# Performance work log

Measured on AMD Instinct MI355X. Metric: run time of the kernel, lower is better.

## Reference

```python
import jax, jax.numpy as jnp
import numpy as np

LEN_HIS = 20   # q_len_his: sliding-window history length
DIM_C = 4      # dim_c
H = 64         # GRU hidden = final_mlp_hidden_width
D = 36         # global_graph_width(32) + goal(2) + action(2)
N = 32768      # total timesteps across many episodes


def setup_inputs() -> dict:
    key = jax.random.key(0)
    ks = jax.random.split(key, 8)
    emb = jax.random.normal(ks[0], (N, D), jnp.float32)
    dones = (jax.random.uniform(ks[1], (N, 1)) < 0.02).astype(jnp.int32)
    s = lambda k, shape, fan: jax.random.normal(k, shape, jnp.float32) / np.sqrt(fan).astype(np.float32)
    return {
        "embeddings": emb,
        "W_ih": s(ks[2], (3 * H, D), D),
        "W_hh": s(ks[3], (3 * H, H), H),
        "b_ih": jnp.zeros((3 * H,), jnp.float32),
        "b_hh": jnp.zeros((3 * H,), jnp.float32),
        "W1": s(ks[4], (H, H), H),
        "b1": jnp.zeros((H,), jnp.float32),
        "W2": s(ks[5], (DIM_C, H), H),
        "b2": jnp.zeros((DIM_C,), jnp.float32),
        "dones": dones,
    }


def _his_calculate_c(embeddings, W_ih, W_hh, b_ih, b_hh, W1, b1, W2, b2, dones):
    """Batched/padded version of the ragged sliding-window GRU+MLP loop.

    For each timestep t, the torch code runs the GRU over
    embeddings[max(episode_start, t-L+1) : t+1] from a zero hidden state,
    then applies FinalPredMLP to the final hidden state.
    """
    n = embeddings.shape[0]
    done = dones[:, 0] != 0
    idx = jnp.arange(n)
    # episode_start[t] = (index of most recent done strictly before t) + 1, else 0
    prev_done = jnp.concatenate([jnp.zeros((1,), bool), done[:-1]])
    ep_start = jax.lax.cummax(jnp.where(prev_done, idx, 0))
    win_start = jnp.maximum(ep_start, idx - LEN_HIS + 1)            # [N]

    # padded windows: position l holds embeddings[t - (L-1) + l]
    gidx = idx[:, None] - (LEN_HIS - 1) + jnp.arange(LEN_HIS)[None, :]  # [N, L]
    valid = gidx >= win_start[:, None]                                   # [N, L]
    X = embeddings[jnp.clip(gidx, 0, n - 1)] * valid[..., None]          # [N, L, D]

    def cell(h, inp):
        x, v = inp                      # x: [N, D], v: [N]
        gi = x @ W_ih.T + b_ih          # [N, 3H]
        gh = h @ W_hh.T + b_hh          # [N, 3H]
        ir, iz, inn = jnp.split(gi, 3, axis=-1)
        hr, hz, hnn = jnp.split(gh, 3, axis=-1)
        r = jax.nn.sigmoid(ir + hr)
        z = jax.nn.sigmoid(iz + hz)
        ncand = jnp.tanh(inn + r * hnn)
        h_new = (1.0 - z) * ncand + z * h
        return jnp.where(v[:, None], h_new, h), None

    h0 = jnp.zeros((n, H), embeddings.dtype)
    hT, _ = jax.lax.scan(cell, h0, (jnp.swapaxes(X, 0, 1), valid.T))  # [N, H]

    # FinalPredMLP: Linear(H,H) -> ReLU -> Linear(H, dim_c)
    hid = jax.nn.relu(hT @ W1.T + b1)
    return hid @ W2.T + b2              # [N, dim_c]


def reference(embeddings, W_ih, W_hh, b_ih, b_hh, W1, b1, W2, b2, dones):
    return _his_calculate_c(embeddings, W_ih, W_hh, b_ih, b_hh, W1, b1, W2, b2, dones)
```

## Files before the change

kernel.cpp:

```cpp
#include <hip/hip_runtime.h>

#define NT 32768
#define DI 36
#define HH 64
#define LH 20
#define TPB 64
#define NROW 83
#define SGS 196
#define EMBS 40

#define NLOG2E -1.4426950408889634f
#define TLOG2E 2.8853900817779268f

#define UNION_OFF  65072
#define SFIRST_OFF 78352
#define SMEM_BYTES 78608

typedef __attribute__((ext_vector_type(8))) short bf16x8;
typedef __attribute__((ext_vector_type(4))) float f32x4;
typedef __attribute__((ext_vector_type(4))) int int4v;
union frag_cast { int4v i4; bf16x8 h8; };

__device__ __forceinline__ unsigned f2u(float f) { union { float f; unsigned u; } x; x.f = f; return x.u; }
__device__ __forceinline__ float u2f(unsigned u) { union { float f; unsigned u; } x; x.u = u; return x.f; }
__device__ __forceinline__ unsigned short f2bf_rne(float f) {
    union { float f; unsigned u; } x; x.f = f;
    unsigned r = x.u + 0x7FFFu + ((x.u >> 16) & 1u);
    return (unsigned short)(r >> 16);
}

__device__ __forceinline__ void gate4(const f32x4 aR, const f32x4 aZ,
                                      const f32x4 aI, const f32x4 aN,
                                      const bool valid, float* hh) {
    float dR[4], dZ[4], dN[4], rv[4], zv[4], iv[4];
#pragma unroll
    for (int e = 0; e < 4; ++e) dR[e] = 1.f + __builtin_amdgcn_exp2f(aR[e]);
#pragma unroll
    for (int e = 0; e < 4; ++e) dZ[e] = 1.f + __builtin_amdgcn_exp2f(aZ[e]);
    {
        const float pa = dR[0] * dR[1], pb = dR[2] * dR[3];
        const float rp = __builtin_amdgcn_rcpf(pa * pb);
        const float ia = rp * pb, ib = rp * pa;
        rv[0] = ia * dR[1]; rv[1] = ia * dR[0];
        rv[2] = ib * dR[3]; rv[3] = ib * dR[2];
    }
    {
        const float pa = dZ[0] * dZ[1], pb = dZ[2] * dZ[3];
        const float rp = __builtin_amdgcn_rcpf(pa * pb);
        const float ia = rp * pb, ib = rp * pa;
        zv[0] = ia * dZ[1]; zv[1] = ia * dZ[0];
        zv[2] = ib * dZ[3]; zv[3] = ib * dZ[2];
    }
#pragma unroll
    for (int e = 0; e < 4; ++e)
        dN[e] = 1.f + __builtin_amdgcn_exp2f(fmaf(rv[e], aN[e], aI[e]));
    {
        const float pa = dN[0] * dN[1], pb = dN[2] * dN[3];
        const float rp = __builtin_amdgcn_rcpf(pa * pb);
        const float ia = rp * pb, ib = rp * pa;
        iv[0] = ia * dN[1]; iv[1] = ia * dN[0];
        iv[2] = ib * dN[3]; iv[3] = ib * dN[2];
    }
#pragma unroll
    for (int e = 0; e < 4; ++e) {
        const float nc = fmaf(-2.f, iv[e], 1.f);
        const float hn = fmaf(zv[e], hh[e] - nc, nc);
        hh[e] = valid ? hn : hh[e];
    }
}

__global__ __launch_bounds__(64) void prep_kernel(
    const float* __restrict__ W_ih, const float* __restrict__ W_hh,
    const float* __restrict__ W1, int4v* __restrict__ wfrag)
{
    const int b = (int)blockIdx.x;
    const int l = (int)threadIdx.x;
    unsigned short e[8];
    if (b < 72) {
        const int set = b / 24, fb = b % 24;
        const int mt = fb >> 1, kt = fb & 1;
        const int m = mt * 16 + (l & 15);
        const float sc = ((mt >> 2) < 2) ? NLOG2E : TLOG2E;
        const int k0 = kt * 32 + (l >> 4) * 8;
#pragma unroll
        for (int jj = 0; jj < 8; ++jj) {
            const int k = k0 + jj;
            if (set == 2) {
                e[jj] = f2bf_rne(W_hh[(size_t)m * HH + k] * sc);
            } else {
                const float v = (k < DI) ? W_ih[(size_t)m * DI + k] * sc : 0.f;
                const unsigned u = f2u(v);
                if (set == 0) e[jj] = (unsigned short)(u >> 16);
                else          e[jj] = (unsigned short)(f2u(v - u2f(u & 0xFFFF0000u)) >> 16);
            }
        }
    } else {
        const int bb = b - 72;
        const bool is_lo = bb >= 8;
        const int f = bb & 7;
        const int mt = f >> 1, kt = f & 1;
        const int m = mt * 16 + (l & 15);
        const int k0 = kt * 32 + (l >> 4) * 8;
#pragma unroll
        for (int jj = 0; jj < 8; ++jj) {
            const float v = W1[(size_t)m * HH + k0 + jj];
            const unsigned u = f2u(v);
            if (!is_lo) e[jj] = (unsigned short)(u >> 16);
            else        e[jj] = (unsigned short)(f2u(v - u2f(u & 0xFFFF0000u)) >> 16);
        }
    }
    int4v p;
    p.x = e[0] | ((unsigned)e[1] << 16); p.y = e[2] | ((unsigned)e[3] << 16);
    p.z = e[4] | ((unsigned)e[5] << 16); p.w = e[6] | ((unsigned)e[7] << 16);
    wfrag[b * 64 + l] = p;
}

__global__ __launch_bounds__(256, 2) void gru_kernel(
    const float* __restrict__ emb, const int4v* __restrict__ wfrag,
    const float* __restrict__ b_ih, const float* __restrict__ b_hh,
    const float* __restrict__ b1, const float* __restrict__ W2,
    const float* __restrict__ b2, const int* __restrict__ dones,
    float* __restrict__ out)
{
    __shared__ __align__(16) char SMEM[SMEM_BYTES];
    float* const Sg = (float*)SMEM;
    unsigned short* const EmbH = (unsigned short*)(SMEM + UNION_OFF);
    unsigned short* const EmbL = EmbH + NROW * EMBS;
    unsigned short* const Hb   = (unsigned short*)(SMEM + UNION_OFF);
    int* const sfirst = (int*)(SMEM + SFIRST_OFF);

    const int tid = threadIdx.x;
    const int lane = tid & 63;
    const int W = tid >> 6;
    const int li = lane & 15;
    const int q = lane >> 4;
    const int blk = ((int)blockIdx.x & 7) * 64 + ((int)blockIdx.x >> 3);
    const int T0 = blk * TPB;

    if (tid < TPB) {
        const int tt = T0 + tid;
        int off = (tt >= LH - 1) ? 0 : (LH - 1) - tt;
#pragma unroll
        for (int k = LH - 1; k >= 1; --k) {
            const int j = tt - k;
            const int jj = j < 0 ? 0 : j;
            const bool d = (j >= 0) && (dones[jj] != 0);
            if (d) off = LH - k;
        }
        sfirst[tid] = off;
    }
    for (int i = tid; i < NROW * 9; i += 256) {
        const int r = i / 9, c = i - r * 9;
        int tt = T0 - (LH - 1) + r; tt = tt < 0 ? 0 : tt;
        const f32x4 v = *(const f32x4*)&emb[(size_t)tt * DI + 4 * c];
        const unsigned u0 = f2u(v[0]), u1 = f2u(v[1]);
        const unsigned u2 = f2u(v[2]), u3 = f2u(v[3]);
        uint2 ph, pl;
        ph.x = __builtin_amdgcn_perm(u1, u0, 0x07060302u);
        ph.y = __builtin_amdgcn_perm(u3, u2, 0x07060302u);
        const unsigned l0 = f2u(v[0] - u2f(u0 & 0xFFFF0000u));
        const unsigned l1 = f2u(v[1] - u2f(u1 & 0xFFFF0000u));
        const unsigned l2 = f2u(v[2] - u2f(u2 & 0xFFFF0000u));
        const unsigned l3 = f2u(v[3] - u2f(u3 & 0xFFFF0000u));
        pl.x = __builtin_amdgcn_perm(l1, l0, 0x07060302u);
        pl.y = __builtin_amdgcn_perm(l3, l2, 0x07060302u);
        *(uint2*)&EmbH[r * EMBS + 4 * c] = ph;
        *(uint2*)&EmbL[r * EMBS + 4 * c] = pl;
    }
    if (tid < NROW) {
        const uint2 z2 = {0u, 0u};
        *(uint2*)&EmbH[tid * EMBS + DI] = z2;
        *(uint2*)&EmbL[tid * EMBS + DI] = z2;
    }

    bf16x8 aih[3][2], ail[3][2];
#pragma unroll
    for (int g = 0; g < 3; ++g)
#pragma unroll
        for (int kt = 0; kt < 2; ++kt) {
            const int fb = (4 * g + W) * 2 + kt;
            frag_cast a, b;
            a.i4 = wfrag[(0 * 24 + fb) * 64 + lane];
            b.i4 = wfrag[(1 * 24 + fb) * 64 + lane];
            aih[g][kt] = a.h8; ail[g][kt] = b.h8;
        }
    bf16x8 whh[3][4][2];
#pragma unroll
    for (int g = 0; g < 3; ++g)
#pragma unroll
        for (int mt = 0; mt < 4; ++mt)
#pragma unroll
            for (int kt = 0; kt < 2; ++kt) {
                frag_cast c;
                c.i4 = wfrag[(48 + (4 * g + mt) * 2 + kt) * 64 + lane];
                whh[g][mt][kt] = c.h8;
            }

    const int joff = 16 * W + 4 * q;
    f32x4 biasI[3];
#pragma unroll
    for (int g = 0; g < 3; ++g) {
        const float sc = (g < 2) ? NLOG2E : TLOG2E;
        const f32x4 bi = *(const f32x4*)&b_ih[64 * g + joff];
        if (g < 2) {
            const f32x4 bh = *(const f32x4*)&b_hh[64 * g + joff];
#pragma unroll
            for (int rr = 0; rr < 4; ++rr) biasI[g][rr] = (bi[rr] + bh[rr]) * sc;
        } else {
#pragma unroll
            for (int rr = 0; rr < 4; ++rr) biasI[g][rr] = bi[rr] * sc;
        }
    }
    __syncthreads();

#pragma unroll
    for (int rt = 0; rt < 6; ++rt) {
        const int row0 = (rt == 5) ? 67 : 16 * rt;
        const int row = row0 + li;
        bf16x8 ebh0 = *(const bf16x8*)&EmbH[row * EMBS + 8 * q];
        bf16x8 ebl0 = *(const bf16x8*)&EmbL[row * EMBS + 8 * q];
        bf16x8 ebh1 = bf16x8{0, 0, 0, 0, 0, 0, 0, 0};
        bf16x8 ebl1 = bf16x8{0, 0, 0, 0, 0, 0, 0, 0};
        if (q == 0) {
            ebh1 = *(const bf16x8*)&EmbH[row * EMBS + 32];
            ebl1 = *(const bf16x8*)&EmbL[row * EMBS + 32];
        }
#pragma unroll
        for (int g = 0; g < 3; ++g) {
            f32x4 a = biasI[g];
            a = __builtin_amdgcn_mfma_f32_16x16x32_bf16(aih[g][0], ebh0, a, 0, 0, 0);
            a = __builtin_amdgcn_mfma_f32_16x16x32_bf16(aih[g][1], ebh1, a, 0, 0, 0);
            a = __builtin_amdgcn_mfma_f32_16x16x32_bf16(ail[g][0], ebh0, a, 0, 0, 0);
            a = __builtin_amdgcn_mfma_f32_16x16x32_bf16(ail[g][1], ebh1, a, 0, 0, 0);
            a = __builtin_amdgcn_mfma_f32_16x16x32_bf16(aih[g][0], ebl0, a, 0, 0, 0);
            a = __builtin_amdgcn_mfma_f32_16x16x32_bf16(aih[g][1], ebl1, a, 0, 0, 0);
            *(f32x4*)&Sg[row * SGS + 64 * g + joff] = a;
        }
    }
    __syncthreads();

    f32x4 bnv4[4];
#pragma unroll
    for (int mt = 0; mt < 4; ++mt) {
        const f32x4 b = *(const f32x4*)&b_hh[128 + 16 * mt + 4 * q];
#pragma unroll
        for (int rr = 0; rr < 4; ++rr) bnv4[mt][rr] = b[rr] * TLOG2E;
    }
    const int sfr = sfirst[16 * W + li];
    unsigned short* const Hbw = Hb + W * 1152;

    float h[4][4];
    f32x4 gvR[4], gvZ[4], gvI[4];
    {
        const float* gp = Sg + (16 * W + li) * SGS;
        const bool valid = (0 >= sfr);
#pragma unroll
        for (int mt = 0; mt < 4; ++mt) {
            const f32x4 aR = *(const f32x4*)(gp + 16 * mt + 4 * q);
            const f32x4 aZ = *(const f32x4*)(gp + 64 + 16 * mt + 4 * q);
            const f32x4 aI = *(const f32x4*)(gp + 128 + 16 * mt + 4 * q);
            h[mt][0] = 0.f; h[mt][1] = 0.f; h[mt][2] = 0.f; h[mt][3] = 0.f;
            gate4(aR, aZ, aI, bnv4[mt], valid, h[mt]);
            uint2 ph;
            ph.x = __builtin_amdgcn_perm(f2u(h[mt][1]), f2u(h[mt][0]), 0x07060302u);
            ph.y = __builtin_amdgcn_perm(f2u(h[mt][3]), f2u(h[mt][2]), 0x07060302u);
            *(uint2*)&Hbw[li * 72 + 16 * mt + 4 * q] = ph;
        }
        const float* gq = Sg + (16 * W + li + 1) * SGS;
#pragma unroll
        for (int mt = 0; mt < 4; ++mt) {
            gvR[mt] = *(const f32x4*)(gq + 16 * mt + 4 * q);
            gvZ[mt] = *(const f32x4*)(gq + 64 + 16 * mt + 4 * q);
            gvI[mt] = *(const f32x4*)(gq + 128 + 16 * mt + 4 * q);
        }
    }

#pragma unroll 2
    for (int s = 1; s < LH; ++s) {
        const bf16x8 bh0 = *(const bf16x8*)&Hbw[li * 72 + 8 * q];
        const bf16x8 bh1 = *(const bf16x8*)&Hbw[li * 72 + 32 + 8 * q];
        f32x4 aR[4], aZ[4], aN[4], aI[4];
#pragma unroll
        for (int mt = 0; mt < 4; ++mt) {
            aR[mt] = gvR[mt]; aZ[mt] = gvZ[mt]; aI[mt] = gvI[mt]; aN[mt] = bnv4[mt];
        }
        {
            int rrow = 16 * W + li + s + 1; rrow = rrow > NROW - 1 ? NROW - 1 : rrow;
            const float* gq = Sg + rrow * SGS;
#pragma unroll
            for (int mt = 0; mt < 4; ++mt) {
                gvR[mt] = *(const f32x4*)(gq + 16 * mt + 4 * q);
                gvZ[mt] = *(const f32x4*)(gq + 64 + 16 * mt + 4 * q);
                gvI[mt] = *(const f32x4*)(gq + 128 + 16 * mt + 4 * q);
            }
        }
        const bool valid = (s >= sfr);
#pragma unroll
        for (int mt = 0; mt < 4; ++mt) {
            aR[mt] = __builtin_amdgcn_mfma_f32_16x16x32_bf16(whh[0][mt][0], bh0, aR[mt], 0, 0, 0);
            aR[mt] = __builtin_amdgcn_mfma_f32_16x16x32_bf16(whh[0][mt][1], bh1, aR[mt], 0, 0, 0);
            aZ[mt] = __builtin_amdgcn_mfma_f32_16x16x32_bf16(whh[1][mt][0], bh0, aZ[mt], 0, 0, 0);
            aZ[mt] = __builtin_amdgcn_mfma_f32_16x16x32_bf16(whh[1][mt][1], bh1, aZ[mt], 0, 0, 0);
            aN[mt] = __builtin_amdgcn_mfma_f32_16x16x32_bf16(whh[2][mt][0], bh0, aN[mt], 0, 0, 0);
            aN[mt] = __builtin_amdgcn_mfma_f32_16x16x32_bf16(whh[2][mt][1], bh1, aN[mt], 0, 0, 0);
            gate4(aR[mt], aZ[mt], aI[mt], aN[mt], valid, h[mt]);
            if (s != LH - 1) {
                uint2 ph;
                ph.x = __builtin_amdgcn_perm(f2u(h[mt][1]), f2u(h[mt][0]), 0x07060302u);
                ph.y = __builtin_amdgcn_perm(f2u(h[mt][3]), f2u(h[mt][2]), 0x07060302u);
                *(uint2*)&Hbw[li * 72 + 16 * mt + 4 * q] = ph;
            }
        }
    }

    bf16x8 w1h[4][2], w1l[4][2];
#pragma unroll
    for (int mt = 0; mt < 4; ++mt)
#pragma unroll
        for (int kt = 0; kt < 2; ++kt) {
            frag_cast a, b;
            a.i4 = wfrag[(72 + mt * 2 + kt) * 64 + lane];
            b.i4 = wfrag[(80 + mt * 2 + kt) * 64 + lane];
            w1h[mt][kt] = a.h8; w1l[mt][kt] = b.h8;
        }
#pragma unroll
    for (int mt = 0; mt < 4; ++mt) {
        uint2 ph;
        ph.x = __builtin_amdgcn_perm(f2u(h[mt][1]), f2u(h[mt][0]), 0x07060302u);
        ph.y = __builtin_amdgcn_perm(f2u(h[mt][3]), f2u(h[mt][2]), 0x07060302u);
        *(uint2*)&Hbw[li * 72 + 16 * mt + 4 * q] = ph;
    }
    const bf16x8 bh0 = *(const bf16x8*)&Hbw[li * 72 + 8 * q];
    const bf16x8 bh1 = *(const bf16x8*)&Hbw[li * 72 + 32 + 8 * q];
#pragma unroll
    for (int mt = 0; mt < 4; ++mt) {
        const unsigned u0 = f2u(h[mt][0]), u1 = f2u(h[mt][1]);
        const unsigned u2 = f2u(h[mt][2]), u3 = f2u(h[mt][3]);
        const unsigned l0 = f2u(h[mt][0] - u2f(u0 & 0xFFFF0000u));
        const unsigned l1 = f2u(h[mt][1] - u2f(u1 & 0xFFFF0000u));
        const unsigned l2 = f2u(h[mt][2] - u2f(u2 & 0xFFFF0000u));
        const unsigned l3 = f2u(h[mt][3] - u2f(u3 & 0xFFFF0000u));
        uint2 pl;
        pl.x = __builtin_amdgcn_perm(l1, l0, 0x07060302u);
        pl.y = __builtin_amdgcn_perm(l3, l2, 0x07060302u);
        *(uint2*)&Hbw[li * 72 + 16 * mt + 4 * q] = pl;
    }
    const bf16x8 bl0 = *(const bf16x8*)&Hbw[li * 72 + 8 * q];
    const bf16x8 bl1 = *(const bf16x8*)&Hbw[li * 72 + 32 + 8 * q];

    float p0 = 0.f, p1 = 0.f, p2 = 0.f, p3 = 0.f;
#pragma unroll
    for (int mt = 0; mt < 4; ++mt) {
        f32x4 a = *(const f32x4*)&b1[16 * mt + 4 * q];
        a = __builtin_amdgcn_mfma_f32_16x16x32_bf16(w1h[mt][0], bh0, a, 0, 0, 0);
        a = __builtin_amdgcn_mfma_f32_16x16x32_bf16(w1h[mt][1], bh1, a, 0, 0, 0);
        a = __builtin_amdgcn_mfma_f32_16x16x32_bf16(w1l[mt][0], bh0, a, 0, 0, 0);
        a = __builtin_amdgcn_mfma_f32_16x16x32_bf16(w1l[mt][1], bh1, a, 0, 0, 0);
        a = __builtin_amdgcn_mfma_f32_16x16x32_bf16(w1h[mt][0], bl0, a, 0, 0, 0);
        a = __builtin_amdgcn_mfma_f32_16x16x32_bf16(w1h[mt][1], bl1, a, 0, 0, 0);
        const float h0 = fmaxf(a[0], 0.f), h1 = fmaxf(a[1], 0.f);
        const float h2 = fmaxf(a[2], 0.f), h3 = fmaxf(a[3], 0.f);
        const f32x4 w0 = *(const f32x4*)&W2[0 * HH + 16 * mt + 4 * q];
        const f32x4 w1 = *(const f32x4*)&W2[1 * HH + 16 * mt + 4 * q];
        const f32x4 w2 = *(const f32x4*)&W2[2 * HH + 16 * mt + 4 * q];
        const f32x4 w3 = *(const f32x4*)&W2[3 * HH + 16 * mt + 4 * q];
        p0 += h0 * w0[0] + h1 * w0[1] + h2 * w0[2] + h3 * w0[3];
        p1 += h0 * w1[0] + h1 * w1[1] + h2 * w1[2] + h3 * w1[3];
        p2 += h0 * w2[0] + h1 * w2[1] + h2 * w2[2] + h3 * w2[3];
        p3 += h0 * w3[0] + h1 * w3[1] + h2 * w3[2] + h3 * w3[3];
    }
    p0 += __shfl_xor(p0, 16); p0 += __shfl_xor(p0, 32);
    p1 += __shfl_xor(p1, 16); p1 += __shfl_xor(p1, 32);
    p2 += __shfl_xor(p2, 16); p2 += __shfl_xor(p2, 32);
    p3 += __shfl_xor(p3, 16); p3 += __shfl_xor(p3, 32);
    const float pv = (q == 0) ? p0 : (q == 1) ? p1 : (q == 2) ? p2 : p3;
    out[(size_t)(T0 + 16 * W + li) * 4 + q] = pv + b2[q];
}

extern "C" void kernel_launch(void* const* d_in, const int* in_sizes, int n_in,
                              void* d_out, int out_size, void* d_ws, size_t ws_size,
                              hipStream_t stream) {
    const float* emb  = (const float*)d_in[0];
    const float* W_ih = (const float*)d_in[1];
    const float* W_hh = (const float*)d_in[2];
    const float* b_ih = (const float*)d_in[3];
    const float* b_hh = (const float*)d_in[4];
    const float* W1   = (const float*)d_in[5];
    const float* b1   = (const float*)d_in[6];
    const float* W2   = (const float*)d_in[7];
    const float* b2   = (const float*)d_in[8];
    const int*   dn   = (const int*)d_in[9];

    int4v* wfrag = (int4v*)d_ws;
    float* o = (float*)d_out;

    prep_kernel<<<88, 64, 0, stream>>>(W_ih, W_hh, W1, wfrag);
    gru_kernel<<<NT / TPB, 256, 0, stream>>>(emb, wfrag, b_ih, b_hh,
                                             b1, W2, b2, dn, o);
}
```

Baseline: 111.4 us.

## Split GRU hidden dimension across two waves per 16-timestep block with fp16 gate staging

Each block now handles 16 timesteps with 128 threads, and the two waves split the 64 hidden units between them instead of each wave owning 16 timesteps with all hidden units. This shrinks the shared memory footprint and per-thread registers so more blocks fit per CU. The precomputed input-gate activations are stored as packed fp16 rather than fp32 to cut LDS usage. The price is a block-wide barrier on every recurrent step to exchange the double-buffered hidden state, an extra LDS reduction for the output head, reduced halo reuse, and lower precision for the staged gate values.

```diff
diff --git a/kernel.cpp b/kernel.cpp
--- a/kernel.cpp
+++ b/kernel.cpp
@@ -4,22 +4,23 @@
 #define DI 36
 #define HH 64
 #define LH 20
-#define TPB 64
-#define NROW 83
-#define SGS 196
+#define TPB 16
+#define NROW 35
+#define SGH 200
 #define EMBS 40
 
 #define NLOG2E -1.4426950408889634f
 #define TLOG2E 2.8853900817779268f
 
-#define UNION_OFF  65072
-#define SFIRST_OFF 78352
-#define SMEM_BYTES 78608
+#define UNION_OFF  14000
+#define SMEM_BYTES 19600
 
 typedef __attribute__((ext_vector_type(8))) short bf16x8;
+typedef __attribute__((ext_vector_type(8))) _Float16 f16x8;
 typedef __attribute__((ext_vector_type(4))) float f32x4;
 typedef __attribute__((ext_vector_type(4))) int int4v;
 union frag_cast { int4v i4; bf16x8 h8; };
+union fh_cast { int4v i4; f16x8 h8; };
 
 __device__ __forceinline__ unsigned f2u(float f) { union { float f; unsigned u; } x; x.f = f; return x.u; }
 __device__ __forceinline__ float u2f(unsigned u) { union { float f; unsigned u; } x; x.u = u; return x.f; }
@@ -27,6 +28,10 @@
     union { float f; unsigned u; } x; x.f = f;
     unsigned r = x.u + 0x7FFFu + ((x.u >> 16) & 1u);
     return (unsigned short)(r >> 16);
+}
+__device__ __forceinline__ unsigned pk2h(float a, float b) {
+    auto h = __builtin_amdgcn_cvt_pkrtz(a, b);
+    union { decltype(h) v; unsigned u; } x; x.v = h; return x.u;
 }
 
 __device__ __forceinline__ void gate4(const f32x4 aR, const f32x4 aZ,
@@ -115,7 +120,7 @@
     wfrag[b * 64 + l] = p;
 }
 
-__global__ __launch_bounds__(256, 2) void gru_kernel(
+__global__ __launch_bounds__(128, 3) void gru_kernel(
     const float* __restrict__ emb, const int4v* __restrict__ wfrag,
     const float* __restrict__ b_ih, const float* __restrict__ b_hh,
     const float* __restrict__ b1, const float* __restrict__ W2,
@@ -123,22 +128,24 @@
     float* __restrict__ out)
 {
     __shared__ __align__(16) char SMEM[SMEM_BYTES];
-    float* const Sg = (float*)SMEM;
+    unsigned short* const Sgh  = (unsigned short*)SMEM;
     unsigned short* const EmbH = (unsigned short*)(SMEM + UNION_OFF);
     unsigned short* const EmbL = EmbH + NROW * EMBS;
     unsigned short* const Hb   = (unsigned short*)(SMEM + UNION_OFF);
-    int* const sfirst = (int*)(SMEM + SFIRST_OFF);
+    float* const red = (float*)SMEM;
 
     const int tid = threadIdx.x;
     const int lane = tid & 63;
     const int W = tid >> 6;
     const int li = lane & 15;
     const int q = lane >> 4;
-    const int blk = ((int)blockIdx.x & 7) * 64 + ((int)blockIdx.x >> 3);
+    const int mtw0 = 2 * W;
+    const int blk = ((int)blockIdx.x & 7) * 256 + ((int)blockIdx.x >> 3);
     const int T0 = blk * TPB;
 
-    if (tid < TPB) {
-        const int tt = T0 + tid;
+    int sfr;
+    {
+        const int tt = T0 + li;
         int off = (tt >= LH - 1) ? 0 : (LH - 1) - tt;
 #pragma unroll
         for (int k = LH - 1; k >= 1; --k) {
@@ -147,9 +154,10 @@
             const bool d = (j >= 0) && (dones[jj] != 0);
             if (d) off = LH - k;
         }
-        sfirst[tid] = off;
-    }
-    for (int i = tid; i < NROW * 9; i += 256) {
+        sfr = off;
+    }
+
+    for (int i = tid; i < NROW * 9; i += 128) {
         const int r = i / 9, c = i - r * 9;
         int tt = T0 - (LH - 1) + r; tt = tt < 0 ? 0 : tt;
         const f32x4 v = *(const f32x4*)&emb[(size_t)tt * DI + 4 * c];
@@ -173,50 +181,29 @@
         *(uint2*)&EmbL[tid * EMBS + DI] = z2;
     }
 
-    bf16x8 aih[3][2], ail[3][2];
-#pragma unroll
-    for (int g = 0; g < 3; ++g)
-#pragma unroll
-        for (int kt = 0; kt < 2; ++kt) {
-            const int fb = (4 * g + W) * 2 + kt;
-            frag_cast a, b;
-            a.i4 = wfrag[(0 * 24 + fb) * 64 + lane];
-            b.i4 = wfrag[(1 * 24 + fb) * 64 + lane];
-            aih[g][kt] = a.h8; ail[g][kt] = b.h8;
-        }
-    bf16x8 whh[3][4][2];
-#pragma unroll
-    for (int g = 0; g < 3; ++g)
-#pragma unroll
-        for (int mt = 0; mt < 4; ++mt)
-#pragma unroll
-            for (int kt = 0; kt < 2; ++kt) {
-                frag_cast c;
-                c.i4 = wfrag[(48 + (4 * g + mt) * 2 + kt) * 64 + lane];
-                whh[g][mt][kt] = c.h8;
-            }
-
-    const int joff = 16 * W + 4 * q;
-    f32x4 biasI[3];
+    f32x4 biasI[3][2];
 #pragma unroll
     for (int g = 0; g < 3; ++g) {
         const float sc = (g < 2) ? NLOG2E : TLOG2E;
-        const f32x4 bi = *(const f32x4*)&b_ih[64 * g + joff];
-        if (g < 2) {
-            const f32x4 bh = *(const f32x4*)&b_hh[64 * g + joff];
-#pragma unroll
-            for (int rr = 0; rr < 4; ++rr) biasI[g][rr] = (bi[rr] + bh[rr]) * sc;
-        } else {
-#pragma unroll
-            for (int rr = 0; rr < 4; ++rr) biasI[g][rr] = bi[rr] * sc;
+#pragma unroll
+        for (int ml = 0; ml < 2; ++ml) {
+            const int jo = 16 * (mtw0 + ml) + 4 * q;
+            const f32x4 bi = *(const f32x4*)&b_ih[64 * g + jo];
+            if (g < 2) {
+                const f32x4 bh = *(const f32x4*)&b_hh[64 * g + jo];
+#pragma unroll
+                for (int rr = 0; rr < 4; ++rr) biasI[g][ml][rr] = (bi[rr] + bh[rr]) * sc;
+            } else {
+#pragma unroll
+                for (int rr = 0; rr < 4; ++rr) biasI[g][ml][rr] = bi[rr] * sc;
+            }
         }
     }
     __syncthreads();
 
 #pragma unroll
-    for (int rt = 0; rt < 6; ++rt) {
-        const int row0 = (rt == 5) ? 67 : 16 * rt;
-        const int row = row0 + li;
+    for (int rt = 0; rt < 3; ++rt) {
+        const int row = ((rt == 2) ? 19 : 16 * rt) + li;
         bf16x8 ebh0 = *(const bf16x8*)&EmbH[row * EMBS + 8 * q];
         bf16x8 ebl0 = *(const bf16x8*)&EmbL[row * EMBS + 8 * q];
         bf16x8 ebh1 = bf16x8{0, 0, 0, 0, 0, 0, 0, 0};
@@ -226,144 +213,159 @@
             ebl1 = *(const bf16x8*)&EmbL[row * EMBS + 32];
         }
 #pragma unroll
-        for (int g = 0; g < 3; ++g) {
-            f32x4 a = biasI[g];
-            a = __builtin_amdgcn_mfma_f32_16x16x32_bf16(aih[g][0], ebh0, a, 0, 0, 0);
-            a = __builtin_amdgcn_mfma_f32_16x16x32_bf16(aih[g][1], ebh1, a, 0, 0, 0);
-            a = __builtin_amdgcn_mfma_f32_16x16x32_bf16(ail[g][0], ebh0, a, 0, 0, 0);
-            a = __builtin_amdgcn_mfma_f32_16x16x32_bf16(ail[g][1], ebh1, a, 0, 0, 0);
-            a = __builtin_amdgcn_mfma_f32_16x16x32_bf16(aih[g][0], ebl0, a, 0, 0, 0);
-            a = __builtin_amdgcn_mfma_f32_16x16x32_bf16(aih[g][1], ebl1, a, 0, 0, 0);
-            *(f32x4*)&Sg[row * SGS + 64 * g + joff] = a;
-        }
+        for (int g = 0; g < 3; ++g)
+#pragma unroll
+            for (int ml = 0; ml < 2; ++ml) {
+                const int fb = (4 * g + mtw0 + ml) * 2;
+                frag_cast a0, a1, c0, c1;
+                a0.i4 = wfrag[(fb + 0) * 64 + lane];
+                a1.i4 = wfrag[(fb + 1) * 64 + lane];
+                c0.i4 = wfrag[(24 + fb + 0) * 64 + lane];
+                c1.i4 = wfrag[(24 + fb + 1) * 64 + lane];
+                f32x4 a = biasI[g][ml];
+                a = __builtin_amdgcn_mfma_f32_16x16x32_bf16(a0.h8, ebh0, a, 0, 0, 0);
+                a = __builtin_amdgcn_mfma_f32_16x16x32_bf16(a1.h8, ebh1, a, 0, 0, 0);
+                a = __builtin_amdgcn_mfma_f32_16x16x32_bf16(c0.h8, ebh0, a, 0, 0, 0);
+                a = __builtin_amdgcn_mfma_f32_16x16x32_bf16(c1.h8, ebh1, a, 0, 0, 0);
+                a = __builtin_amdgcn_mfma_f32_16x16x32_bf16(a0.h8, ebl0, a, 0, 0, 0);
+                a = __builtin_amdgcn_mfma_f32_16x16x32_bf16(a1.h8, ebl1, a, 0, 0, 0);
+                uint2 pk;
+                pk.x = pk2h(a[0], a[1]);
+                pk.y = pk2h(a[2], a[3]);
+                *(uint2*)&Sgh[row * SGH + W * 96 + q * 24 + g * 8 + ml * 4] = pk;
+            }
     }
     __syncthreads();
 
-    f32x4 bnv4[4];
-#pragma unroll
-    for (int mt = 0; mt < 4; ++mt) {
-        const f32x4 b = *(const f32x4*)&b_hh[128 + 16 * mt + 4 * q];
-#pragma unroll
-        for (int rr = 0; rr < 4; ++rr) bnv4[mt][rr] = b[rr] * TLOG2E;
-    }
-    const int sfr = sfirst[16 * W + li];
-    unsigned short* const Hbw = Hb + W * 1152;
-
-    float h[4][4];
-    f32x4 gvR[4], gvZ[4], gvI[4];
+    bf16x8 whh[3][2][2];
+#pragma unroll
+    for (int g = 0; g < 3; ++g)
+#pragma unroll
+        for (int ml = 0; ml < 2; ++ml)
+#pragma unroll
+            for (int kt = 0; kt < 2; ++kt) {
+                frag_cast c;
+                c.i4 = wfrag[(48 + (4 * g + mtw0 + ml) * 2 + kt) * 64 + lane];
+                whh[g][ml][kt] = c.h8;
+            }
+    f32x4 bnv[2];
+#pragma unroll
+    for (int ml = 0; ml < 2; ++ml) {
+        const f32x4 b = *(const f32x4*)&b_hh[128 + 16 * (mtw0 + ml) + 4 * q];
+#pragma unroll
+        for (int rr = 0; rr < 4; ++rr) bnv[ml][rr] = b[rr] * TLOG2E;
+    }
+    const int gbase = W * 96 + q * 24;
+
+    float h[2][4];
     {
-        const float* gp = Sg + (16 * W + li) * SGS;
+        fh_cast cR, cZ, cI;
+        cR.i4 = *(const int4v*)&Sgh[li * SGH + gbase + 0];
+        cZ.i4 = *(const int4v*)&Sgh[li * SGH + gbase + 8];
+        cI.i4 = *(const int4v*)&Sgh[li * SGH + gbase + 16];
         const bool valid = (0 >= sfr);
 #pragma unroll
-        for (int mt = 0; mt < 4; ++mt) {
-            const f32x4 aR = *(const f32x4*)(gp + 16 * mt + 4 * q);
-            const f32x4 aZ = *(const f32x4*)(gp + 64 + 16 * mt + 4 * q);
-            const f32x4 aI = *(const f32x4*)(gp + 128 + 16 * mt + 4 * q);
-            h[mt][0] = 0.f; h[mt][1] = 0.f; h[mt][2] = 0.f; h[mt][3] = 0.f;
-            gate4(aR, aZ, aI, bnv4[mt], valid, h[mt]);
+        for (int ml = 0; ml < 2; ++ml) {
+            f32x4 aR, aZ, aI;
+#pragma unroll
+            for (int rr = 0; rr < 4; ++rr) {
+                aR[rr] = (float)cR.h8[4 * ml + rr];
+                aZ[rr] = (float)cZ.h8[4 * ml + rr];
+                aI[rr] = (float)cI.h8[4 * ml + rr];
+            }
+            h[ml][0] = 0.f; h[ml][1] = 0.f; h[ml][2] = 0.f; h[ml][3] = 0.f;
+            gate4(aR, aZ, aI, bnv[ml], valid, h[ml]);
             uint2 ph;
-            ph.x = __builtin_amdgcn_perm(f2u(h[mt][1]), f2u(h[mt][0]), 0x07060302u);
-            ph.y = __builtin_amdgcn_perm(f2u(h[mt][3]), f2u(h[mt][2]), 0x07060302u);
-            *(uint2*)&Hbw[li * 72 + 16 * mt + 4 * q] = ph;
-        }
-        const float* gq = Sg + (16 * W + li + 1) * SGS;
-#pragma unroll
-        for (int mt = 0; mt < 4; ++mt) {
-            gvR[mt] = *(const f32x4*)(gq + 16 * mt + 4 * q);
-            gvZ[mt] = *(const f32x4*)(gq + 64 + 16 * mt + 4 * q);
-            gvI[mt] = *(const f32x4*)(gq + 128 + 16 * mt + 4 * q);
-        }
-    }
+            ph.x = __builtin_amdgcn_perm(f2u(h[ml][1]), f2u(h[ml][0]), 0x07060302u);
+            ph.y = __builtin_amdgcn_perm(f2u(h[ml][3]), f2u(h[ml][2]), 0x07060302u);
+            *(uint2*)&Hb[li * 72 + 16 * (mtw0 + ml) + 4 * q] = ph;
+        }
+    }
+    __syncthreads();
 
 #pragma unroll 2
     for (int s = 1; s < LH; ++s) {
-        const bf16x8 bh0 = *(const bf16x8*)&Hbw[li * 72 + 8 * q];
-        const bf16x8 bh1 = *(const bf16x8*)&Hbw[li * 72 + 32 + 8 * q];
-        f32x4 aR[4], aZ[4], aN[4], aI[4];
-#pragma unroll
-        for (int mt = 0; mt < 4; ++mt) {
-            aR[mt] = gvR[mt]; aZ[mt] = gvZ[mt]; aI[mt] = gvI[mt]; aN[mt] = bnv4[mt];
-        }
-        {
-            int rrow = 16 * W + li + s + 1; rrow = rrow > NROW - 1 ? NROW - 1 : rrow;
-            const float* gq = Sg + rrow * SGS;
-#pragma unroll
-            for (int mt = 0; mt < 4; ++mt) {
-                gvR[mt] = *(const f32x4*)(gq + 16 * mt + 4 * q);
-                gvZ[mt] = *(const f32x4*)(gq + 64 + 16 * mt + 4 * q);
-                gvI[mt] = *(const f32x4*)(gq + 128 + 16 * mt + 4 * q);
-            }
+        const int rb = (s + 1) & 1;
+        const bf16x8 bh0 = *(const bf16x8*)&Hb[rb * 1152 + li * 72 + 8 * q];
+        const bf16x8 bh1 = *(const bf16x8*)&Hb[rb * 1152 + li * 72 + 32 + 8 * q];
+        fh_cast cR, cZ, cI;
+        const int gro = (li + s) * SGH + gbase;
+        cR.i4 = *(const int4v*)&Sgh[gro + 0];
+        cZ.i4 = *(const int4v*)&Sgh[gro + 8];
+        cI.i4 = *(const int4v*)&Sgh[gro + 16];
+        f32x4 aR[2], aZ[2], aI[2], aN[2];
+#pragma unroll
+        for (int ml = 0; ml < 2; ++ml) {
+#pragma unroll
+            for (int rr = 0; rr < 4; ++rr) {
+                aR[ml][rr] = (float)cR.h8[4 * ml + rr];
+                aZ[ml][rr] = (float)cZ.h8[4 * ml + rr];
+                aI[ml][rr] = (float)cI.h8[4 * ml + rr];
+            }
+            aN[ml] = bnv[ml];
+        }
+#pragma unroll
+        for (int ml = 0; ml < 2; ++ml) {
+            aR[ml] = __builtin_amdgcn_mfma_f32_16x16x32_bf16(whh[0][ml][0], bh0, aR[ml], 0, 0, 0);
+            aR[ml] = __builtin_amdgcn_mfma_f32_16x16x32_bf16(whh[0][ml][1], bh1, aR[ml], 0, 0, 0);
+            aZ[ml] = __builtin_amdgcn_mfma_f32_16x16x32_bf16(whh[1][ml][0], bh0, aZ[ml], 0, 0, 0);
+            aZ[ml] = __builtin_amdgcn_mfma_f32_16x16x32_bf16(whh[1][ml][1], bh1, aZ[ml], 0, 0, 0);
+            aN[ml] = __builtin_amdgcn_mfma_f32_16x16x32_bf16(whh[2][ml][0], bh0, aN[ml], 0, 0, 0);
+            aN[ml] = __builtin_amdgcn_mfma_f32_16x16x32_bf16(whh[2][ml][1], bh1, aN[ml], 0, 0, 0);
         }
         const bool valid = (s >= sfr);
 #pragma unroll
-        for (int mt = 0; mt < 4; ++mt) {
-            aR[mt] = __builtin_amdgcn_mfma_f32_16x16x32_bf16(whh[0][mt][0], bh0, aR[mt], 0, 0, 0);
-            aR[mt] = __builtin_amdgcn_mfma_f32_16x16x32_bf16(whh[0][mt][1], bh1, aR[mt], 0, 0, 0);
-            aZ[mt] = __builtin_amdgcn_mfma_f32_16x16x32_bf16(whh[1][mt][0], bh0, aZ[mt], 0, 0, 0);
-            aZ[mt] = __builtin_amdgcn_mfma_f32_16x16x32_bf16(whh[1][mt][1], bh1, aZ[mt], 0, 0, 0);
-            aN[mt] = __builtin_amdgcn_mfma_f32_16x16x32_bf16(whh[2][mt][0], bh0, aN[mt], 0, 0, 0);
-            aN[mt] = __builtin_amdgcn_mfma_f32_16x16x32_bf16(whh[2][mt][1], bh1, aN[mt], 0, 0, 0);
-            gate4(aR[mt], aZ[mt], aI[mt], aN[mt], valid, h[mt]);
-            if (s != LH - 1) {
-                uint2 ph;
-                ph.x = __builtin_amdgcn_perm(f2u(h[mt][1]), f2u(h[mt][0]), 0x07060302u);
-                ph.y = __builtin_amdgcn_perm(f2u(h[mt][3]), f2u(h[mt][2]), 0x07060302u);
-                *(uint2*)&Hbw[li * 72 + 16 * mt + 4 * q] = ph;
-            }
-        }
-    }
-
-    bf16x8 w1h[4][2], w1l[4][2];
-#pragma unroll
-    for (int mt = 0; mt < 4; ++mt)
-#pragma unroll
-        for (int kt = 0; kt < 2; ++kt) {
-            frag_cast a, b;
-            a.i4 = wfrag[(72 + mt * 2 + kt) * 64 + lane];
-            b.i4 = wfrag[(80 + mt * 2 + kt) * 64 + lane];
-            w1h[mt][kt] = a.h8; w1l[mt][kt] = b.h8;
-        }
-#pragma unroll
-    for (int mt = 0; mt < 4; ++mt) {
-        uint2 ph;
-        ph.x = __builtin_amdgcn_perm(f2u(h[mt][1]), f2u(h[mt][0]), 0x07060302u);
-        ph.y = __builtin_amdgcn_perm(f2u(h[mt][3]), f2u(h[mt][2]), 0x07060302u);
-        *(uint2*)&Hbw[li * 72 + 16 * mt + 4 * q] = ph;
-    }
-    const bf16x8 bh0 = *(const bf16x8*)&Hbw[li * 72 + 8 * q];
-    const bf16x8 bh1 = *(const bf16x8*)&Hbw[li * 72 + 32 + 8 * q];
-#pragma unroll
-    for (int mt = 0; mt < 4; ++mt) {
-        const unsigned u0 = f2u(h[mt][0]), u1 = f2u(h[mt][1]);
-        const unsigned u2 = f2u(h[mt][2]), u3 = f2u(h[mt][3]);
-        const unsigned l0 = f2u(h[mt][0] - u2f(u0 & 0xFFFF0000u));
-        const unsigned l1 = f2u(h[mt][1] - u2f(u1 & 0xFFFF0000u));
-        const unsigned l2 = f2u(h[mt][2] - u2f(u2 & 0xFFFF0000u));
-        const unsigned l3 = f2u(h[mt][3] - u2f(u3 & 0xFFFF0000u));
+        for (int ml = 0; ml < 2; ++ml) {
+            gate4(aR[ml], aZ[ml], aI[ml], aN[ml], valid, h[ml]);
+            uint2 ph;
+            ph.x = __builtin_amdgcn_perm(f2u(h[ml][1]), f2u(h[ml][0]), 0x07060302u);
+            ph.y = __builtin_amdgcn_perm(f2u(h[ml][3]), f2u(h[ml][2]), 0x07060302u);
+            *(uint2*)&Hb[(s & 1) * 1152 + li * 72 + 16 * (mtw0 + ml) + 4 * q] = ph;
+        }
+        __syncthreads();
+    }
+
+#pragma unroll
+    for (int ml = 0; ml < 2; ++ml) {
+        const unsigned u0 = f2u(h[ml][0]), u1 = f2u(h[ml][1]);
+        const unsigned u2 = f2u(h[ml][2]), u3 = f2u(h[ml][3]);
+        const unsigned l0 = f2u(h[ml][0] - u2f(u0 & 0xFFFF0000u));
+        const unsigned l1 = f2u(h[ml][1] - u2f(u1 & 0xFFFF0000u));
+        const unsigned l2 = f2u(h[ml][2] - u2f(u2 & 0xFFFF0000u));
+        const unsigned l3 = f2u(h[ml][3] - u2f(u3 & 0xFFFF0000u));
         uint2 pl;
         pl.x = __builtin_amdgcn_perm(l1, l0, 0x07060302u);
         pl.y = __builtin_amdgcn_perm(l3, l2, 0x07060302u);
-        *(uint2*)&Hbw[li * 72 + 16 * mt + 4 * q] = pl;
-    }
-    const bf16x8 bl0 = *(const bf16x8*)&Hbw[li * 72 + 8 * q];
-    const bf16x8 bl1 = *(const bf16x8*)&Hbw[li * 72 + 32 + 8 * q];
+        *(uint2*)&Hb[li * 72 + 16 * (mtw0 + ml) + 4 * q] = pl;
+    }
+    __syncthreads();
+    const bf16x8 bh0 = *(const bf16x8*)&Hb[1152 + li * 72 + 8 * q];
+    const bf16x8 bh1 = *(const bf16x8*)&Hb[1152 + li * 72 + 32 + 8 * q];
+    const bf16x8 bl0 = *(const bf16x8*)&Hb[li * 72 + 8 * q];
+    const bf16x8 bl1 = *(const bf16x8*)&Hb[li * 72 + 32 + 8 * q];
 
     float p0 = 0.f, p1 = 0.f, p2 = 0.f, p3 = 0.f;
 #pragma unroll
-    for (int mt = 0; mt < 4; ++mt) {
-        f32x4 a = *(const f32x4*)&b1[16 * mt + 4 * q];
-        a = __builtin_amdgcn_mfma_f32_16x16x32_bf16(w1h[mt][0], bh0, a, 0, 0, 0);
-        a = __builtin_amdgcn_mfma_f32_16x16x32_bf16(w1h[mt][1], bh1, a, 0, 0, 0);
-        a = __builtin_amdgcn_mfma_f32_16x16x32_bf16(w1l[mt][0], bh0, a, 0, 0, 0);
-        a = __builtin_amdgcn_mfma_f32_16x16x32_bf16(w1l[mt][1], bh1, a, 0, 0, 0);
-        a = __builtin_amdgcn_mfma_f32_16x16x32_bf16(w1h[mt][0], bl0, a, 0, 0, 0);
-        a = __builtin_amdgcn_mfma_f32_16x16x32_bf16(w1h[mt][1], bl1, a, 0, 0, 0);
+    for (int ml = 0; ml < 2; ++ml) {
+        frag_cast w1h0, w1h1, w1l0, w1l1;
+        w1h0.i4 = wfrag[(72 + (mtw0 + ml) * 2 + 0) * 64 + lane];
+        w1h1.i4 = wfrag[(72 + (mtw0 + ml) * 2 + 1) * 64 + lane];
+        w1l0.i4 = wfrag[(80 + (mtw0 + ml) * 2 + 0) * 64 + lane];
+        w1l1.i4 = wfrag[(80 + (mtw0 + ml) * 2 + 1) * 64 + lane];
+        f32x4 a = *(const f32x4*)&b1[16 * (mtw0 + ml) + 4 * q];
+        a = __builtin_amdgcn_mfma_f32_16x16x32_bf16(w1h0.h8, bh0, a, 0, 0, 0);
+        a = __builtin_amdgcn_mfma_f32_16x16x32_bf16(w1h1.h8, bh1, a, 0, 0, 0);
+        a = __builtin_amdgcn_mfma_f32_16x16x32_bf16(w1l0.h8, bh0, a, 0, 0, 0);
+        a = __builtin_amdgcn_mfma_f32_16x16x32_bf16(w1l1.h8, bh1, a, 0, 0, 0);
+        a = __builtin_amdgcn_mfma_f32_16x16x32_bf16(w1h0.h8, bl0, a, 0, 0, 0);
+        a = __builtin_amdgcn_mfma_f32_16x16x32_bf16(w1h1.h8, bl1, a, 0, 0, 0);
         const float h0 = fmaxf(a[0], 0.f), h1 = fmaxf(a[1], 0.f);
         const float h2 = fmaxf(a[2], 0.f), h3 = fmaxf(a[3], 0.f);
-        const f32x4 w0 = *(const f32x4*)&W2[0 * HH + 16 * mt + 4 * q];
-        const f32x4 w1 = *(const f32x4*)&W2[1 * HH + 16 * mt + 4 * q];
-        const f32x4 w2 = *(const f32x4*)&W2[2 * HH + 16 * mt + 4 * q];
-        const f32x4 w3 = *(const f32x4*)&W2[3 * HH + 16 * mt + 4 * q];
+        const int mo = 16 * (mtw0 + ml) + 4 * q;
+        const f32x4 w0 = *(const f32x4*)&W2[0 * HH + mo];
+        const f32x4 w1 = *(const f32x4*)&W2[1 * HH + mo];
+        const f32x4 w2 = *(const f32x4*)&W2[2 * HH + mo];
+        const f32x4 w3 = *(const f32x4*)&W2[3 * HH + mo];
         p0 += h0 * w0[0] + h1 * w0[1] + h2 * w0[2] + h3 * w0[3];
         p1 += h0 * w1[0] + h1 * w1[1] + h2 * w1[2] + h3 * w1[3];
         p2 += h0 * w2[0] + h1 * w2[1] + h2 * w2[2] + h3 * w2[3];
@@ -374,7 +376,10 @@
     p2 += __shfl_xor(p2, 16); p2 += __shfl_xor(p2, 32);
     p3 += __shfl_xor(p3, 16); p3 += __shfl_xor(p3, 32);
     const float pv = (q == 0) ? p0 : (q == 1) ? p1 : (q == 2) ? p2 : p3;
-    out[(size_t)(T0 + 16 * W + li) * 4 + q] = pv + b2[q];
+    red[W * 64 + li * 4 + q] = pv;
+    __syncthreads();
+    if (W == 0)
+        out[(size_t)(T0 + li) * 4 + q] = red[li * 4 + q] + red[64 + li * 4 + q] + b2[q];
 }
 
 extern "C" void kernel_launch(void* const* d_in, const int* in_sizes, int n_in,
@@ -385,7 +390,6 @@
     const float* W_hh = (const float*)d_in[2];
     const float* b_ih = (const float*)d_in[3];
     const float* b_hh = (const float*)d_in[4];
-    const float* W1   = (const float*)d_in[5];
     const float* b1   = (const float*)d_in[6];
     const float* W2   = (const float*)d_in[7];
     const float* b2   = (const float*)d_in[8];
@@ -394,7 +398,7 @@
     int4v* wfrag = (int4v*)d_ws;
     float* o = (float*)d_out;
 
-    prep_kernel<<<88, 64, 0, stream>>>(W_ih, W_hh, W1, wfrag);
-    gru_kernel<<<NT / TPB, 256, 0, stream>>>(emb, wfrag, b_ih, b_hh,
+    prep_kernel<<<88, 64, 0, stream>>>(W_ih, W_hh, (const float*)d_in[5], wfrag);
+    gru_kernel<<<NT / TPB, 128, 0, stream>>>(emb, wfrag, b_ih, b_hh,
                                              b1, W2, b2, dn, o);
 }
```

After: 131.0 us. +17.6%, slower.
